# Kernel tuning notes

Hardware: AMD Instinct MI355X
Metric: run time of the kernel (lower is better)

## Reference

```python
import jax, jax.numpy as jnp
import numpy as np

B, N, L, D = 4, 128, 20, 512


def setup_inputs() -> dict:
    key = jax.random.key(0)
    ks = jax.random.split(key, 8)
    return {
        "f_b": jax.random.normal(ks[0], (B, N, D), jnp.float32),
        "f_w": jax.random.normal(ks[1], (B, L, D), jnp.float32),
        "f_s": jax.random.normal(ks[2], (B, D), jnp.float32),
        "f_m": jax.random.normal(ks[3], (B, N, N, D), jnp.float32),
        "Wq": jax.random.normal(ks[4], (D, D), jnp.float32) / np.sqrt(D).astype(np.float32),
        "bq": jax.random.normal(ks[5], (D,), jnp.float32) * 0.02,
        "Wk": jax.random.normal(ks[6], (D, D), jnp.float32) / np.sqrt(D).astype(np.float32),
        "bk": jax.random.normal(ks[7], (D,), jnp.float32) * 0.02,
    }


def reference(f_b, f_w, f_s, f_m, Wq, bq, Wk, bk):
    d = f_b.shape[-1]
    scale = jnp.asarray(1.0 / np.sqrt(d), f_b.dtype)
    # cross-attention: boundary features attend to word features
    q = f_b @ Wq.T + bq                                   # [B,N,D]
    k = f_w @ Wk.T + bk                                   # [B,L,D]
    attn = jax.nn.softmax(jnp.einsum('bnd,bld->bnl', q, k) * scale, axis=-1)
    f_baq = jnp.einsum('bnl,bld->bnd', attn, f_w)         # [B,N,D]
    # sentence-gated boundary features
    f_bq = f_b * (f_baq + f_s[:, None, :])                # [B,N,D]
    # boundary self-attention
    A_b = jax.nn.softmax(jnp.einsum('bnd,bmd->bnm', f_bq, f_bq) * scale, axis=-1)
    f_bb = jnp.einsum('bnm,bmd->bnd', A_b, f_b)           # [B,N,D]
    # gated moment-map reduction: sum_i A_b[b,i,j] * sigmoid(f_m*f_s)*f_m
    g_m = jax.nn.sigmoid(f_m * f_s[:, None, None, :])     # [B,N,N,D]
    f_bm = jnp.einsum('bij,bijd->bjd', A_b, g_m * f_m)    # [B,N,D]
    return f_bb + f_b + f_bm
```

## Files before the change

### kernel.cpp

```cpp
#include <hip/hip_runtime.h>
#include <hip/hip_bf16.h>

#define Bc 4
#define Nc 128
#define Lc 20
#define Dc 512
#define SCALE 0.04419417382415922f
#define NL2E -1.4426950408889634f

#if __has_builtin(__builtin_amdgcn_exp2f)
#define EXP2(x) __builtin_amdgcn_exp2f(x)
#else
#define EXP2(x) __expf((x) * 0.6931471805599453f)
#endif

typedef float vf4 __attribute__((ext_vector_type(4)));

#if __has_builtin(__builtin_nontemporal_load)
#define NT_LOAD4(p) __builtin_nontemporal_load((const vf4*)(p))
#else
#define NT_LOAD4(p) (*(const vf4*)(p))
#endif

__global__ __launch_bounds__(256)
void proj_gemm(const float* __restrict__ f_b, const float* __restrict__ f_w,
               const float* __restrict__ Wq, const float* __restrict__ bq,
               const float* __restrict__ Wk, const float* __restrict__ bk,
               float* __restrict__ qb, float* __restrict__ kb) {
    const int t  = threadIdx.x;
    const int tr = blockIdx.y, tc = blockIdx.x, kh = blockIdx.z;
    const int c0 = tc * 32;
    const bool isq = tr < 16;
    const float* Ain  = isq ? f_b : f_w;
    const float* W    = isq ? Wq : Wk;
    const float* bias = isq ? bq : bk;
    float* C          = isq ? (qb + kh * 512 * Dc) : (kb + kh * 80 * Dc);
    const int r0    = isq ? tr * 32 : (tr - 16) * 32;
    const int nrows = isq ? 512 : 80;
    const int kbase = kh * 128;

    __shared__ __align__(16) float As[16 * 34];
    __shared__ __align__(16) float Bs[16 * 34];

    const int sr  = t >> 3;
    const int sk2 = (t & 7) * 2;
    const int arow = min(r0 + sr, nrows - 1);
    const int wrow = c0 + sr;

    const int ty2 = (t >> 4) * 2;
    const int tx2 = (t & 15) * 2;
    float a00 = 0.f, a01 = 0.f, a10 = 0.f, a11 = 0.f;

    const float* Aptr = Ain + arow * Dc + kbase + sk2;
    const float* Wptr = W   + wrow * Dc + kbase + sk2;
    float2 ga = *(const float2*)Aptr;
    float2 gb = *(const float2*)Wptr;

    for (int kk0 = 16; kk0 <= 128; kk0 += 16) {
        __syncthreads();
        As[sk2 * 34 + sr]       = ga.x;
        As[(sk2 + 1) * 34 + sr] = ga.y;
        Bs[sk2 * 34 + sr]       = gb.x;
        Bs[(sk2 + 1) * 34 + sr] = gb.y;
        __syncthreads();
        if (kk0 < 128) {
            ga = *(const float2*)(Aptr + kk0);
            gb = *(const float2*)(Wptr + kk0);
        }
#pragma unroll
        for (int kk = 0; kk < 16; kk++) {
            const float2 av = *(const float2*)&As[kk * 34 + ty2];
            const float2 bv = *(const float2*)&Bs[kk * 34 + tx2];
            a00 = fmaf(av.x, bv.x, a00); a01 = fmaf(av.x, bv.y, a01);
            a10 = fmaf(av.y, bv.x, a10); a11 = fmaf(av.y, bv.y, a11);
        }
    }
    const int orow = r0 + ty2;
    const float b0 = kh ? 0.f : bias[c0 + tx2];
    const float b1 = kh ? 0.f : bias[c0 + tx2 + 1];
    if (orow < nrows)
        *(float2*)&C[orow * Dc + c0 + tx2] = make_float2(a00 + b0, a01 + b1);
    if (orow + 1 < nrows)
        *(float2*)&C[(orow + 1) * Dc + c0 + tx2] = make_float2(a10 + b0, a11 + b1);
}

__global__ __launch_bounds__(256)
void cross_attn_gate(const float* __restrict__ qb, const float* __restrict__ kb,
                     const float* __restrict__ f_w, const float* __restrict__ f_b,
                     const float* __restrict__ f_s, float* __restrict__ f_bq) {
    const int bn = blockIdx.x;
    const int b  = bn >> 7;
    const int t  = threadIdx.x;
    const int lane = t & 63, wave = t >> 6;

    __shared__ __align__(16) float qs[Dc];
    __shared__ float sc[32];
    __shared__ float invs;

    {
        float2 s = make_float2(0.f, 0.f);
#pragma unroll
        for (int h = 0; h < 4; h++) {
            const float2 u = ((const float2*)(qb + h * 512 * Dc + bn * Dc))[t];
            s.x += u.x; s.y += u.y;
        }
        ((float2*)qs)[t] = s;
    }
    __syncthreads();

    const float4* q4 = (const float4*)qs;
    const float4 qa = q4[lane];
    const float4 qv = q4[lane + 64];

    for (int l = wave; l < Lc; l += 4) {
        float4 ka = make_float4(0.f, 0.f, 0.f, 0.f);
        float4 kv = make_float4(0.f, 0.f, 0.f, 0.f);
#pragma unroll
        for (int h = 0; h < 4; h++) {
            const float4* kr = (const float4*)(kb + h * 80 * Dc + (b * Lc + l) * Dc);
            const float4 u = kr[lane];
            const float4 v = kr[lane + 64];
            ka.x += u.x; ka.y += u.y; ka.z += u.z; ka.w += u.w;
            kv.x += v.x; kv.y += v.y; kv.z += v.z; kv.w += v.w;
        }
        float s = qa.x * ka.x + qa.y * ka.y + qa.z * ka.z + qa.w * ka.w
                + qv.x * kv.x + qv.y * kv.y + qv.z * kv.z + qv.w * kv.w;
#pragma unroll
        for (int d = 32; d >= 1; d >>= 1) s += __shfl_down(s, d, 64);
        if (lane == 0) sc[l] = s * SCALE;
    }
    __syncthreads();

    if (t == 0) {
        float mx = sc[0];
        for (int l = 1; l < Lc; l++) mx = fmaxf(mx, sc[l]);
        float sum = 0.f;
        for (int l = 0; l < Lc; l++) { float e = __expf(sc[l] - mx); sc[l] = e; sum += e; }
        invs = 1.0f / sum;
    }
    __syncthreads();
    const float inv = invs;

    const float2* fw2 = (const float2*)(f_w + b * Lc * Dc);
    float2 acc = make_float2(0.f, 0.f);
#pragma unroll 5
    for (int l = 0; l < Lc; l++) {
        const float2 v = fw2[l * 256 + t];
        const float w = sc[l];
        acc.x = fmaf(w, v.x, acc.x);
        acc.y = fmaf(w, v.y, acc.y);
    }
    const float2 s2 = ((const float2*)(f_s + b * Dc))[t];
    const float2 fb2 = ((const float2*)(f_b + bn * Dc))[t];
    float2 o;
    o.x = fb2.x * (acc.x * inv + s2.x);
    o.y = fb2.y * (acc.y * inv + s2.y);
    ((float2*)(f_bq + bn * Dc))[t] = o;
}

__global__ __launch_bounds__(512)
void self_attn_scores(const float* __restrict__ f_bq,
                      float* __restrict__ A_b, float* __restrict__ A_bT) {
    const int bn = blockIdx.x;
    const int b  = bn >> 7, n = bn & 127;
    const int t  = threadIdx.x;
    const int lane = t & 63, wave = t >> 6;

    __shared__ __align__(16) float qrow[Dc];
    __shared__ float sc[Nc];
    __shared__ float redm[2];
    __shared__ float reds[2];

    qrow[t] = f_bq[bn * Dc + t];
    __syncthreads();

    const float4* q4 = (const float4*)qrow;
    const float4 qa = q4[lane];
    const float4 qv = q4[lane + 64];

    for (int m = wave; m < Nc; m += 8) {
        const float4* kr = (const float4*)(f_bq + (b * Nc + m) * Dc);
        const float4 va = kr[lane];
        const float4 vb = kr[lane + 64];
        float s = qa.x * va.x + qa.y * va.y + qa.z * va.z + qa.w * va.w
                + qv.x * vb.x + qv.y * vb.y + qv.z * vb.z + qv.w * vb.w;
#pragma unroll
        for (int d = 32; d >= 1; d >>= 1) s += __shfl_down(s, d, 64);
        if (lane == 0) sc[m] = s * SCALE;
    }
    __syncthreads();

    float sval = 0.f, e = 0.f;
    if (t < Nc) {
        sval = sc[t];
        float m = sval;
#pragma unroll
        for (int d = 32; d >= 1; d >>= 1) m = fmaxf(m, __shfl_xor(m, d, 64));
        if (lane == 0) redm[wave] = m;
    }
    __syncthreads();
    if (t < Nc) {
        const float mx = fmaxf(redm[0], redm[1]);
        e = __expf(sval - mx);
        float s = e;
#pragma unroll
        for (int d = 32; d >= 1; d >>= 1) s += __shfl_xor(s, d, 64);
        if (lane == 0) reds[wave] = s;
    }
    __syncthreads();
    if (t < Nc) {
        const float a = e * (1.0f / (reds[0] + reds[1]));
        A_b[bn * Nc + t] = a;
        A_bT[(b * Nc + t) * Nc + n] = a;
    }
}

__global__ __launch_bounds__(256, 4)
void moment_final(const float* __restrict__ f_m, const float* __restrict__ f_s,
                  const float* __restrict__ A_b, const float* __restrict__ A_bT,
                  const float* __restrict__ f_b, float* __restrict__ out) {
    const int bj = blockIdx.x;
    const int b  = bj >> 7, j = bj & 127;
    const int dh = blockIdx.y;
    const int t  = threadIdx.x;
    const int c  = t & 63;
    const int g  = t >> 6;

    __shared__ float w[Nc];
    __shared__ float ar[Nc];
    __shared__ __align__(16) float4 pex[3][64];

    if (t < Nc) w[t] = A_bT[bj * Nc + t];
    else        ar[t - Nc] = A_b[bj * Nc + (t - Nc)];
    __syncthreads();

    const int c4 = dh * 64 + c;
    const float4 s4 = ((const float4*)(f_s + b * Dc))[c4];
    const float4 ns = make_float4(NL2E * s4.x, NL2E * s4.y, NL2E * s4.z, NL2E * s4.w);

    float4 acc = make_float4(0.f, 0.f, 0.f, 0.f);
    const float* fm = f_m;
    const long istride = (long)Nc * Dc;
    long idx = ((long)(b * Nc + g * 32) * Nc + j) * Dc + c4 * 4;

#pragma unroll 1
    for (int ii = 0; ii < 32; ii += 8) {
        vf4 mv[8];
#pragma unroll
        for (int u = 0; u < 8; u++)
            mv[u] = NT_LOAD4(fm + idx + (long)u * istride);
        idx += 8 * istride;
#pragma unroll
        for (int u = 0; u < 8; u++) {
            const float ww = w[g * 32 + ii + u];
            const vf4 m4 = mv[u];
            acc.x = fmaf(ww * m4.x, __builtin_amdgcn_rcpf(1.f + EXP2(m4.x * ns.x)), acc.x);
            acc.y = fmaf(ww * m4.y, __builtin_amdgcn_rcpf(1.f + EXP2(m4.y * ns.y)), acc.y);
            acc.z = fmaf(ww * m4.z, __builtin_amdgcn_rcpf(1.f + EXP2(m4.z * ns.z)), acc.z);
            acc.w = fmaf(ww * m4.w, __builtin_amdgcn_rcpf(1.f + EXP2(m4.w * ns.w)), acc.w);
        }
    }

    const float4* fb4 = (const float4*)(f_b + b * Nc * Dc);
    const int mbase = g * 32;
#pragma unroll 4
    for (int m = mbase; m < mbase + 32; m++) {
        const float a = ar[m];
        const float4 v = fb4[m * (Dc / 4) + c4];
        acc.x = fmaf(a, v.x, acc.x); acc.y = fmaf(a, v.y, acc.y);
        acc.z = fmaf(a, v.z, acc.z); acc.w = fmaf(a, v.w, acc.w);
    }

    if (g != 0) pex[g - 1][c] = acc;
    __syncthreads();
    if (g == 0) {
#pragma unroll
        for (int p = 0; p < 3; p++) {
            const float4 q = pex[p][c];
            acc.x += q.x; acc.y += q.y; acc.z += q.z; acc.w += q.w;
        }
        const float4 r = fb4[j * (Dc / 4) + c4];
        acc.x += r.x; acc.y += r.y; acc.z += r.z; acc.w += r.w;
        ((float4*)out)[bj * (Dc / 4) + c4] = acc;
    }
}

extern "C" void kernel_launch(void* const* d_in, const int* in_sizes, int n_in,
                              void* d_out, int out_size, void* d_ws, size_t ws_size,
                              hipStream_t stream) {
    const float* f_b = (const float*)d_in[0];
    const float* f_w = (const float*)d_in[1];
    const float* f_s = (const float*)d_in[2];
    const float* f_m = (const float*)d_in[3];
    const float* Wq  = (const float*)d_in[4];
    const float* bq  = (const float*)d_in[5];
    const float* Wk  = (const float*)d_in[6];
    const float* bk  = (const float*)d_in[7];
    float* out = (float*)d_out;

    float* ws   = (float*)d_ws;
    float* qb   = ws;
    float* kb   = qb   + 4 * 512 * Dc;
    float* f_bq = kb   + 4 * 80 * Dc;
    float* A_b  = f_bq + 512 * Dc;
    float* A_bT = A_b  + 512 * Nc;

    proj_gemm<<<dim3(16, 19, 4), 256, 0, stream>>>(f_b, f_w, Wq, bq, Wk, bk, qb, kb);
    cross_attn_gate<<<Bc * Nc, 256, 0, stream>>>(qb, kb, f_w, f_b, f_s, f_bq);
    self_attn_scores<<<Bc * Nc, 512, 0, stream>>>(f_bq, A_b, A_bT);
    moment_final<<<dim3(Bc * Nc, 2), 256, 0, stream>>>(f_m, f_s, A_b, A_bT, f_b, out);
}
```

Before: 236.9 us.

## Enlarge projection GEMM tiles to 64x64 with 4x4 register blocking

Rewrites the Q/K projection GEMM to use 64x64 output tiles with a 4x4 per-thread accumulator and float4 global loads, and changes the split-K layout to 8 slices for Q and 4 for K. Larger tiles are meant to raise arithmetic intensity and cut shared-memory traffic per FMA. The cross-attention kernel now sums 8 Q partials, which adds some extra partial-sum traffic. Blocks for the K rows beyond slice 4 exit immediately, which wastes some launch slots.

```diff
diff --git a/kernel.cpp b/kernel.cpp
--- a/kernel.cpp
+++ b/kernel.cpp
@@ -28,60 +28,82 @@
                const float* __restrict__ Wk, const float* __restrict__ bk,
                float* __restrict__ qb, float* __restrict__ kb) {
     const int t  = threadIdx.x;
-    const int tr = blockIdx.y, tc = blockIdx.x, kh = blockIdx.z;
-    const int c0 = tc * 32;
-    const bool isq = tr < 16;
+    const int tc = blockIdx.x, ty = blockIdx.y, kz = blockIdx.z;
+    const bool isq = ty < 8;
+    if (!isq && kz >= 4) return;
+    const int c0    = tc * 64;
+    const int r0    = isq ? ty * 64 : (ty - 8) * 64;
+    const int nrows = isq ? 512 : 80;
+    const int KB    = isq ? 64 : 128;
+    const int kbase = isq ? kz * 64 : kz * 128;
     const float* Ain  = isq ? f_b : f_w;
     const float* W    = isq ? Wq : Wk;
     const float* bias = isq ? bq : bk;
-    float* C          = isq ? (qb + kh * 512 * Dc) : (kb + kh * 80 * Dc);
-    const int r0    = isq ? tr * 32 : (tr - 16) * 32;
-    const int nrows = isq ? 512 : 80;
-    const int kbase = kh * 128;
-
-    __shared__ __align__(16) float As[16 * 34];
-    __shared__ __align__(16) float Bs[16 * 34];
-
-    const int sr  = t >> 3;
-    const int sk2 = (t & 7) * 2;
-    const int arow = min(r0 + sr, nrows - 1);
-    const int wrow = c0 + sr;
-
-    const int ty2 = (t >> 4) * 2;
-    const int tx2 = (t & 15) * 2;
-    float a00 = 0.f, a01 = 0.f, a10 = 0.f, a11 = 0.f;
-
-    const float* Aptr = Ain + arow * Dc + kbase + sk2;
-    const float* Wptr = W   + wrow * Dc + kbase + sk2;
-    float2 ga = *(const float2*)Aptr;
-    float2 gb = *(const float2*)Wptr;
-
-    for (int kk0 = 16; kk0 <= 128; kk0 += 16) {
+    float* C          = isq ? (qb + kz * 512 * Dc) : (kb + kz * 80 * Dc);
+
+    __shared__ __align__(16) float As[16][68];
+    __shared__ __align__(16) float Bs[16][68];
+
+    const int srow = t >> 2;
+    const int sk4  = (t & 3) * 4;
+    const int arow = min(r0 + srow, nrows - 1);
+    const int wrow = c0 + srow;
+
+    const int rr = (t >> 4) * 4;
+    const int cc = (t & 15) * 4;
+    float acc[4][4] = {};
+
+    const float* Aptr = Ain + arow * Dc + kbase + sk4;
+    const float* Wptr = W   + wrow * Dc + kbase + sk4;
+    float4 ga = *(const float4*)Aptr;
+    float4 gb = *(const float4*)Wptr;
+
+    for (int kk0 = 16; kk0 <= KB; kk0 += 16) {
         __syncthreads();
-        As[sk2 * 34 + sr]       = ga.x;
-        As[(sk2 + 1) * 34 + sr] = ga.y;
-        Bs[sk2 * 34 + sr]       = gb.x;
-        Bs[(sk2 + 1) * 34 + sr] = gb.y;
+        As[sk4 + 0][srow] = ga.x; As[sk4 + 1][srow] = ga.y;
+        As[sk4 + 2][srow] = ga.z; As[sk4 + 3][srow] = ga.w;
+        Bs[sk4 + 0][srow] = gb.x; Bs[sk4 + 1][srow] = gb.y;
+        Bs[sk4 + 2][srow] = gb.z; Bs[sk4 + 3][srow] = gb.w;
         __syncthreads();
-        if (kk0 < 128) {
-            ga = *(const float2*)(Aptr + kk0);
-            gb = *(const float2*)(Wptr + kk0);
+        if (kk0 < KB) {
+            ga = *(const float4*)(Aptr + kk0);
+            gb = *(const float4*)(Wptr + kk0);
         }
 #pragma unroll
         for (int kk = 0; kk < 16; kk++) {
-            const float2 av = *(const float2*)&As[kk * 34 + ty2];
-            const float2 bv = *(const float2*)&Bs[kk * 34 + tx2];
-            a00 = fmaf(av.x, bv.x, a00); a01 = fmaf(av.x, bv.y, a01);
-            a10 = fmaf(av.y, bv.x, a10); a11 = fmaf(av.y, bv.y, a11);
-        }
-    }
-    const int orow = r0 + ty2;
-    const float b0 = kh ? 0.f : bias[c0 + tx2];
-    const float b1 = kh ? 0.f : bias[c0 + tx2 + 1];
-    if (orow < nrows)
-        *(float2*)&C[orow * Dc + c0 + tx2] = make_float2(a00 + b0, a01 + b1);
-    if (orow + 1 < nrows)
-        *(float2*)&C[(orow + 1) * Dc + c0 + tx2] = make_float2(a10 + b0, a11 + b1);
+            const float4 av = *(const float4*)&As[kk][rr];
+            const float4 bv = *(const float4*)&Bs[kk][cc];
+            acc[0][0] = fmaf(av.x, bv.x, acc[0][0]);
+            acc[0][1] = fmaf(av.x, bv.y, acc[0][1]);
+            acc[0][2] = fmaf(av.x, bv.z, acc[0][2]);
+            acc[0][3] = fmaf(av.x, bv.w, acc[0][3]);
+            acc[1][0] = fmaf(av.y, bv.x, acc[1][0]);
+            acc[1][1] = fmaf(av.y, bv.y, acc[1][1]);
+            acc[1][2] = fmaf(av.y, bv.z, acc[1][2]);
+            acc[1][3] = fmaf(av.y, bv.w, acc[1][3]);
+            acc[2][0] = fmaf(av.z, bv.x, acc[2][0]);
+            acc[2][1] = fmaf(av.z, bv.y, acc[2][1]);
+            acc[2][2] = fmaf(av.z, bv.z, acc[2][2]);
+            acc[2][3] = fmaf(av.z, bv.w, acc[2][3]);
+            acc[3][0] = fmaf(av.w, bv.x, acc[3][0]);
+            acc[3][1] = fmaf(av.w, bv.y, acc[3][1]);
+            acc[3][2] = fmaf(av.w, bv.z, acc[3][2]);
+            acc[3][3] = fmaf(av.w, bv.w, acc[3][3]);
+        }
+    }
+
+    float4 bv4 = make_float4(0.f, 0.f, 0.f, 0.f);
+    if (kz == 0) bv4 = *(const float4*)&bias[c0 + cc];
+#pragma unroll
+    for (int i = 0; i < 4; i++) {
+        const int orow = r0 + rr + i;
+        if (orow < nrows) {
+            float4 o;
+            o.x = acc[i][0] + bv4.x; o.y = acc[i][1] + bv4.y;
+            o.z = acc[i][2] + bv4.z; o.w = acc[i][3] + bv4.w;
+            *(float4*)&C[orow * Dc + c0 + cc] = o;
+        }
+    }
 }
 
 __global__ __launch_bounds__(256)
@@ -100,7 +122,7 @@
     {
         float2 s = make_float2(0.f, 0.f);
 #pragma unroll
-        for (int h = 0; h < 4; h++) {
+        for (int h = 0; h < 8; h++) {
             const float2 u = ((const float2*)(qb + h * 512 * Dc + bn * Dc))[t];
             s.x += u.x; s.y += u.y;
         }
@@ -300,12 +322,12 @@
 
     float* ws   = (float*)d_ws;
     float* qb   = ws;
-    float* kb   = qb   + 4 * 512 * Dc;
+    float* kb   = qb   + 8 * 512 * Dc;
     float* f_bq = kb   + 4 * 80 * Dc;
     float* A_b  = f_bq + 512 * Dc;
     float* A_bT = A_b  + 512 * Nc;
 
-    proj_gemm<<<dim3(16, 19, 4), 256, 0, stream>>>(f_b, f_w, Wq, bq, Wk, bk, qb, kb);
+    proj_gemm<<<dim3(8, 10, 8), 256, 0, stream>>>(f_b, f_w, Wq, bq, Wk, bk, qb, kb);
     cross_attn_gate<<<Bc * Nc, 256, 0, stream>>>(qb, kb, f_w, f_b, f_s, f_bq);
     self_attn_scores<<<Bc * Nc, 512, 0, stream>>>(f_bq, A_b, A_bT);
     moment_final<<<dim3(Bc * Nc, 2), 256, 0, stream>>>(f_m, f_s, A_b, A_bT, f_b, out);
```

Result: no change. 234.1 us (median of 2 runs) (-1.2%).
